# Kernel optimization log

Measured on AMD Instinct MI355X. Metric: run time of the kernel, lower is better.

The kernel has to match this reference:

```python
import jax, jax.numpy as jnp
import numpy as np

N_NODES = 100000
N_EDGES = 1600000
IN_FEATS = 256
OUT_FEATS = 128


def setup_inputs() -> dict:
    key = jax.random.key(0)
    k1, k2, k3, k4, k5 = jax.random.split(key, 5)
    feat = jax.random.normal(k1, (N_NODES, IN_FEATS), dtype=jnp.float32)
    # xavier_uniform-like init for the weight
    limit = float(np.sqrt(6.0 / (IN_FEATS + OUT_FEATS)))
    weight = jax.random.uniform(k2, (IN_FEATS, OUT_FEATS), dtype=jnp.float32,
                                minval=-limit, maxval=limit)
    edge_weight = jax.random.uniform(k3, (N_EDGES,), dtype=jnp.float32)
    src = jax.random.randint(k4, (N_EDGES,), 0, N_NODES, dtype=jnp.int64)
    dst = jax.random.randint(k5, (N_EDGES,), 0, N_NODES, dtype=jnp.int64)
    return {"feat": feat, "weight": weight, "edge_weight": edge_weight,
            "src": src, "dst": dst}


def reference(feat, weight, edge_weight, src, dst):
    N = feat.shape[0]
    ones = jnp.ones(src.shape, dtype=feat.dtype)
    # out/in degrees from edge list (clamped to >= 1), as in DGL
    out_deg = jnp.clip(jax.ops.segment_sum(ones, src, num_segments=N), 1.0)
    in_deg = jnp.clip(jax.ops.segment_sum(ones, dst, num_segments=N), 1.0)
    # norm == 'both': pre-scale sources by out_deg^-0.5
    feat_src = feat * (out_deg ** -0.5)[:, None]
    # in_feats > out_feats branch: transform (with tanh) BEFORE aggregation
    h = jnp.tanh(feat_src @ weight)                      # [N, out]
    # message = u_mul_e: h[src] * edge_weight, then sum per destination
    m = h[src] * edge_weight[:, None]                    # [E, out]
    rst = jax.ops.segment_sum(m, dst, num_segments=N)    # [N, out]
    # norm == 'both': post-scale by in_deg^-0.5
    rst = rst * (in_deg ** -0.5)[:, None]
    return rst
```

## Files before the change

kernel.cpp:

```cpp
#include <hip/hip_runtime.h>
#include <hip/hip_fp16.h>
#include <math.h>

#define N_NODES 100000
#define N_EDGES 1600000
#define IN_F 256
#define OUT_F 128
#define SCAN_TPB 256
#define SCAN_EPB 1024

#define HR 4
#define HRANGE 25000
#define HC 64
#define HCHUNK 25000
#define PWORDS (N_NODES / 2)

typedef _Float16 h8 __attribute__((ext_vector_type(8)));
typedef float f4 __attribute__((ext_vector_type(4)));

__global__ __launch_bounds__(256) void hist_kernel(
        const int* __restrict__ src, const int* __restrict__ dst,
        int* __restrict__ rank, unsigned int* __restrict__ partial_in,
        unsigned int* __restrict__ partial_out) {
    __shared__ unsigned int bins[HRANGE / 2];
    int b = blockIdx.x;
    int c = b >> 3;
    int tr = b & 7;
    int type = tr >> 2;
    int r = tr & 3;
    for (int i = threadIdx.x; i < HRANGE / 2; i += 256) bins[i] = 0;
    __syncthreads();
    const int* nodes = type ? src : dst;
    const int e0 = c * HCHUNK;
    const int lo = r * HRANGE;
    const int ngroups = HCHUNK / 4;
    for (int g = threadIdx.x; g < ngroups; g += 256) {
        int e = e0 + g * 4;
        int4 n4 = *(const int4*)(nodes + e);
        int nn[4] = {n4.x, n4.y, n4.z, n4.w};
        #pragma unroll
        for (int j = 0; j < 4; ++j) {
            unsigned loc = (unsigned)(nn[j] - lo);
            if (loc < (unsigned)HRANGE) {
                unsigned sh = (loc & 1) * 16;
                unsigned old = atomicAdd(&bins[loc >> 1], 1u << sh);
                if (type == 0) rank[e + j] = (int)((old >> sh) & 0xffffu);
            }
        }
    }
    __syncthreads();
    unsigned int* part = type ? partial_out : partial_in;
    unsigned int* dstp = part + (size_t)c * PWORDS + (lo >> 1);
    for (int i = threadIdx.x; i < HRANGE / 2; i += 256) dstp[i] = bins[i];
}

__global__ __launch_bounds__(256) void fused_reduce_kernel(
        const unsigned int* __restrict__ partial_in,
        const unsigned int* __restrict__ partial_out,
        unsigned short* __restrict__ chunk_base16,
        int* __restrict__ deg_in, float* __restrict__ rs_out,
        int* __restrict__ spart, int N) {
    __shared__ int tmp[256];
    int t = threadIdx.x;
    int n0 = blockIdx.x * SCAN_EPB + t * 4;
    int run[4] = {0, 0, 0, 0};
    int sout[4] = {0, 0, 0, 0};
    if (n0 < N) {
        const int w0 = n0 >> 1;
        #pragma unroll 4
        for (int c = 0; c < HC; ++c) {
            ushort4 cb;
            cb.x = (unsigned short)run[0]; cb.y = (unsigned short)run[1];
            cb.z = (unsigned short)run[2]; cb.w = (unsigned short)run[3];
            *(ushort4*)(chunk_base16 + (size_t)c * N_NODES + n0) = cb;
            uint2 pi = *(const uint2*)(partial_in + (size_t)c * PWORDS + w0);
            run[0] += (int)(pi.x & 0xffffu);  run[1] += (int)(pi.x >> 16);
            run[2] += (int)(pi.y & 0xffffu);  run[3] += (int)(pi.y >> 16);
            uint2 po = *(const uint2*)(partial_out + (size_t)c * PWORDS + w0);
            sout[0] += (int)(po.x & 0xffffu); sout[1] += (int)(po.x >> 16);
            sout[2] += (int)(po.y & 0xffffu); sout[3] += (int)(po.y >> 16);
        }
        *(int4*)(deg_in + n0) = make_int4(run[0], run[1], run[2], run[3]);
        float4 rs;
        rs.x = rsqrtf((float)(sout[0] < 1 ? 1 : sout[0]));
        rs.y = rsqrtf((float)(sout[1] < 1 ? 1 : sout[1]));
        rs.z = rsqrtf((float)(sout[2] < 1 ? 1 : sout[2]));
        rs.w = rsqrtf((float)(sout[3] < 1 ? 1 : sout[3]));
        *(float4*)(rs_out + n0) = rs;
    }
    tmp[t] = run[0] + run[1] + run[2] + run[3];
    __syncthreads();
    for (int off = 128; off > 0; off >>= 1) {
        if (t < off) tmp[t] += tmp[t + off];
        __syncthreads();
    }
    if (t == 0) spart[blockIdx.x] = tmp[0];
}

__global__ __launch_bounds__(128) void scan_part2(const int* __restrict__ partials,
                                                  int* __restrict__ bases, int nb) {
    __shared__ int tmp[128];
    int t = threadIdx.x;
    int v = (t < nb) ? partials[t] : 0;
    tmp[t] = v;
    __syncthreads();
    int x = v;
    for (int off = 1; off < 128; off <<= 1) {
        int y = (t >= off) ? tmp[t - off] : 0;
        __syncthreads();
        x += y;
        tmp[t] = x;
        __syncthreads();
    }
    if (t < nb) bases[t] = x - v;
}

__global__ __launch_bounds__(SCAN_TPB) void scan_part3(const int* __restrict__ deg,
                                                       const int* __restrict__ bases,
                                                       int* __restrict__ row_ptr, int N) {
    __shared__ int tmp[SCAN_TPB];
    int t = threadIdx.x;
    int i0 = blockIdx.x * SCAN_EPB + t * 4;
    int v[4];
    int s = 0;
    #pragma unroll
    for (int j = 0; j < 4; ++j) { v[j] = (i0 + j < N) ? deg[i0 + j] : 0; s += v[j]; }
    tmp[t] = s;
    __syncthreads();
    int x = s;
    for (int off = 1; off < SCAN_TPB; off <<= 1) {
        int y = (t >= off) ? tmp[t - off] : 0;
        __syncthreads();
        x += y;
        tmp[t] = x;
        __syncthreads();
    }
    int excl = bases[blockIdx.x] + x - s;
    #pragma unroll
    for (int j = 0; j < 4; ++j) {
        if (i0 + j < N) row_ptr[i0 + j] = excl;
        excl += v[j];
    }
    if (blockIdx.x == gridDim.x - 1 && t == SCAN_TPB - 1) row_ptr[N] = bases[blockIdx.x] + x;
}

__global__ __launch_bounds__(256) void fill_kernel(
        const int* __restrict__ src, const int* __restrict__ dst,
        const float* __restrict__ ew, const int* __restrict__ row_ptr,
        const unsigned short* __restrict__ chunk_base16,
        const int* __restrict__ rank, int2* __restrict__ ed, int E) {
    int e0 = (blockIdx.x * 256 + threadIdx.x) * 4;
    if (e0 >= E) return;
    int4 s4 = *(const int4*)(src + e0);
    int4 d4 = *(const int4*)(dst + e0);
    float4 w4 = *(const float4*)(ew + e0);
    int4 r4 = *(const int4*)(rank + e0);
    int c = e0 / HCHUNK;
    const unsigned short* cb = chunk_base16 + (size_t)c * N_NODES;
    int dd[4] = {d4.x, d4.y, d4.z, d4.w};
    int ss[4] = {s4.x, s4.y, s4.z, s4.w};
    int rr[4] = {r4.x, r4.y, r4.z, r4.w};
    float ww[4] = {w4.x, w4.y, w4.z, w4.w};
    #pragma unroll
    for (int j = 0; j < 4; ++j) {
        int d = dd[j];
        int p = row_ptr[d] + (int)cb[d] + rr[j];
        unsigned long long v = (unsigned long long)(unsigned int)ss[j] |
                               ((unsigned long long)(unsigned int)__float_as_int(ww[j]) << 32);
        __builtin_nontemporal_store(v, (unsigned long long*)&ed[p]);
    }
}

__global__ void wt_kernel(const float* __restrict__ W, _Float16* __restrict__ Wt) {
    int i = blockIdx.x * blockDim.x + threadIdx.x;
    if (i < IN_F * OUT_F) {
        int n = i >> 8;
        int k = i & 255;
        Wt[i] = (_Float16)W[k * OUT_F + n];
    }
}

__global__ __launch_bounds__(256) void gemm_mfma_kernel(
        const float* __restrict__ feat, const _Float16* __restrict__ Wt,
        const float* __restrict__ rs_out, __half* __restrict__ h, int N) {
    const int wave = threadIdx.x >> 6;
    const int lane = threadIdx.x & 63;
    const int m = lane & 15;
    const int quad = lane >> 4;
    const int n0 = wave * 32;

    h8 b[2][8];
    #pragma unroll
    for (int t = 0; t < 2; ++t)
        #pragma unroll
        for (int k = 0; k < 8; ++k)
            b[t][k] = *(const h8*)&Wt[(size_t)(n0 + t * 16 + m) * IN_F + k * 32 + quad * 8];

    const int rowbase = blockIdx.x * 64;

    #pragma unroll
    for (int pair = 0; pair < 2; ++pair) {
        const int r0 = rowbase + pair * 32;
        int ar0 = r0 + m;       if (ar0 >= N) ar0 = 0;
        int ar1 = r0 + 16 + m;  if (ar1 >= N) ar1 = 0;
        const float* ap0 = feat + (size_t)ar0 * IN_F + quad * 8;
        const float* ap1 = feat + (size_t)ar1 * IN_F + quad * 8;

        f4 acc00 = {0.f, 0.f, 0.f, 0.f}, acc01 = {0.f, 0.f, 0.f, 0.f};
        f4 acc10 = {0.f, 0.f, 0.f, 0.f}, acc11 = {0.f, 0.f, 0.f, 0.f};

        #pragma unroll
        for (int k = 0; k < 8; ++k) {
            float4 f00 = *(const float4*)(ap0 + k * 32);
            float4 f01 = *(const float4*)(ap0 + k * 32 + 4);
            float4 f10 = *(const float4*)(ap1 + k * 32);
            float4 f11 = *(const float4*)(ap1 + k * 32 + 4);
            h8 a0, a1;
            a0[0] = (_Float16)f00.x; a0[1] = (_Float16)f00.y;
            a0[2] = (_Float16)f00.z; a0[3] = (_Float16)f00.w;
            a0[4] = (_Float16)f01.x; a0[5] = (_Float16)f01.y;
            a0[6] = (_Float16)f01.z; a0[7] = (_Float16)f01.w;
            a1[0] = (_Float16)f10.x; a1[1] = (_Float16)f10.y;
            a1[2] = (_Float16)f10.z; a1[3] = (_Float16)f10.w;
            a1[4] = (_Float16)f11.x; a1[5] = (_Float16)f11.y;
            a1[6] = (_Float16)f11.z; a1[7] = (_Float16)f11.w;
            acc00 = __builtin_amdgcn_mfma_f32_16x16x32_f16(a0, b[0][k], acc00, 0, 0, 0);
            acc01 = __builtin_amdgcn_mfma_f32_16x16x32_f16(a0, b[1][k], acc01, 0, 0, 0);
            acc10 = __builtin_amdgcn_mfma_f32_16x16x32_f16(a1, b[0][k], acc10, 0, 0, 0);
            acc11 = __builtin_amdgcn_mfma_f32_16x16x32_f16(a1, b[1][k], acc11, 0, 0, 0);
        }

        #pragma unroll
        for (int tile = 0; tile < 2; ++tile) {
            const f4 aL = tile ? acc10 : acc00;
            const f4 aR = tile ? acc11 : acc01;
            const int crow = r0 + tile * 16 + quad * 4;
            #pragma unroll
            for (int r = 0; r < 4; ++r) {
                const int rr = crow + r;
                if (rr < N) {
                    const float rs = rs_out[rr];
                    h[(size_t)rr * OUT_F + n0 + m]      = __float2half(tanhf(aL[r] * rs));
                    h[(size_t)rr * OUT_F + n0 + 16 + m] = __float2half(tanhf(aR[r] * rs));
                }
            }
        }
    }
}

__global__ __launch_bounds__(256) void gather_kernel(
        const __half* __restrict__ h, const int2* __restrict__ ed,
        const int* __restrict__ row_ptr, float* __restrict__ out, int N) {
    int wave = threadIdx.x >> 6;
    int lane = threadIdx.x & 63;
    int node = blockIdx.x * 4 + wave;
    if (node >= N) return;
    int lo = row_ptr[node];
    int hi = row_ptr[node + 1];
    int p = lane >> 4;
    int c = lane & 15;
    float acc[4][8];
    #pragma unroll
    for (int g = 0; g < 4; ++g)
        #pragma unroll
        for (int i = 0; i < 8; ++i) acc[g][i] = 0.f;

    for (int j = lo; j < hi; j += 16) {
        #pragma unroll
        for (int g = 0; g < 4; ++g) {
            int jj = j + g * 4 + p;
            int2 e = (jj < hi) ? ed[jj] : make_int2(0, 0);
            float w = __int_as_float(e.y);
            int4 rrow = *(const int4*)(h + (size_t)e.x * OUT_F + c * 8);
            float2 t;
            t = __half22float2(*(__half2*)&rrow.x); acc[g][0] += w * t.x; acc[g][1] += w * t.y;
            t = __half22float2(*(__half2*)&rrow.y); acc[g][2] += w * t.x; acc[g][3] += w * t.y;
            t = __half22float2(*(__half2*)&rrow.z); acc[g][4] += w * t.x; acc[g][5] += w * t.y;
            t = __half22float2(*(__half2*)&rrow.w); acc[g][6] += w * t.x; acc[g][7] += w * t.y;
        }
    }
    float v[8];
    #pragma unroll
    for (int i = 0; i < 8; ++i) {
        v[i] = (acc[0][i] + acc[1][i]) + (acc[2][i] + acc[3][i]);
        v[i] += __shfl_xor(v[i], 16);
        v[i] += __shfl_xor(v[i], 32);
    }
    if (p == 0) {
        int deg = hi - lo; if (deg < 1) deg = 1;
        float rs = rsqrtf((float)deg);
        float* op = out + (size_t)node * OUT_F + c * 8;
        *(float4*)op       = make_float4(v[0] * rs, v[1] * rs, v[2] * rs, v[3] * rs);
        *(float4*)(op + 4) = make_float4(v[4] * rs, v[5] * rs, v[6] * rs, v[7] * rs);
    }
}

extern "C" void kernel_launch(void* const* d_in, const int* in_sizes, int n_in,
                              void* d_out, int out_size, void* d_ws, size_t ws_size,
                              hipStream_t stream) {
    const float* feat   = (const float*)d_in[0];
    const float* weight = (const float*)d_in[1];
    const float* ew     = (const float*)d_in[2];
    const int*   src    = (const int*)d_in[3];
    const int*   dst    = (const int*)d_in[4];
    float* out = (float*)d_out;

    char* ws = (char*)d_ws;
    float* rs_out      = (float*)(ws);
    int*   deg_in      = (int*)(ws + 400000);
    int*   row_ptr     = (int*)(ws + 800000);
    int*   spart       = (int*)(ws + 1200016);
    int*   sbases      = (int*)(ws + 1200528);
    int*   rank        = (int*)(ws + 1201056);
    unsigned int* partial_in  = (unsigned int*)(ws + 7601056);
    int2*  ed          = (int2*)(ws + 7601056);
    unsigned short* chunk_base16 = (unsigned short*)(ws + 20401056);
    unsigned int* partial_out = (unsigned int*)(ws + 33201056);
    __half* h          = (__half*)(ws + 20401056);
    _Float16* Wt       = (_Float16*)(ws + 46001056);

    const int nb = (N_NODES + SCAN_EPB - 1) / SCAN_EPB;

    hist_kernel<<<2 * HR * HC, 256, 0, stream>>>(src, dst, rank, partial_in, partial_out);
    fused_reduce_kernel<<<nb, 256, 0, stream>>>(partial_in, partial_out, chunk_base16,
                                                deg_in, rs_out, spart, N_NODES);
    scan_part2<<<1, 128, 0, stream>>>(spart, sbases, nb);
    scan_part3<<<nb, SCAN_TPB, 0, stream>>>(deg_in, sbases, row_ptr, N_NODES);
    fill_kernel<<<(N_EDGES / 4 + 255) / 256, 256, 0, stream>>>(src, dst, ew, row_ptr,
                                                               chunk_base16, rank, ed, N_EDGES);
    wt_kernel<<<(IN_F * OUT_F + 255) / 256, 256, 0, stream>>>(weight, Wt);
    gemm_mfma_kernel<<<(N_NODES + 63) / 64, 256, 0, stream>>>(feat, Wt, rs_out, h, N_NODES);
    gather_kernel<<<(N_NODES + 3) / 4, 256, 0, stream>>>(h, ed, row_ptr, out, N_NODES);
}
```

Baseline: 403.0 us.

## Stage GEMM weights in swizzled LDS and process 128 rows per block

The fp16 transposed weight matrix (64 KB) is now copied into LDS with an XOR swizzle, instead of each wave holding 16 h8 B fragments in registers. Each block now handles 128 rows, as two halves of 64 rows with four A tiles per wave, which halves the number of blocks and spreads the weight load over more rows. B fragments are read from LDS on every k step. The goal is lower register pressure (launch bounds 256,2) and more rows in flight per wave to hide feat loads, at the cost of a 64 KB LDS footprint that limits occupancy and a per-block weight staging prologue.

```diff
diff --git a/kernel.cpp b/kernel.cpp
--- a/kernel.cpp
+++ b/kernel.cpp
@@ -14,6 +14,8 @@
 #define HC 64
 #define HCHUNK 25000
 #define PWORDS (N_NODES / 2)
+
+#define GM_ROWS 128
 
 typedef _Float16 h8 __attribute__((ext_vector_type(8)));
 typedef float f4 __attribute__((ext_vector_type(4)));
@@ -180,42 +182,72 @@
     }
 }
 
-__global__ __launch_bounds__(256) void gemm_mfma_kernel(
+__global__ __launch_bounds__(256, 2) void gemm_mfma_kernel(
         const float* __restrict__ feat, const _Float16* __restrict__ Wt,
         const float* __restrict__ rs_out, __half* __restrict__ h, int N) {
-    const int wave = threadIdx.x >> 6;
-    const int lane = threadIdx.x & 63;
+    __shared__ _Float16 wlds[OUT_F * IN_F];
+    const int tid = threadIdx.x;
+
+    for (int gi = tid; gi < OUT_F * IN_F / 8; gi += 256) {
+        int row = gi >> 5;
+        int gc  = gi & 31;
+        int gs  = gc ^ (row & 7);
+        *(int4*)&wlds[(size_t)(row * 32 + gs) * 8] = *(const int4*)&Wt[(size_t)gi * 8];
+    }
+    __syncthreads();
+
+    const int wave = tid >> 6;
+    const int lane = tid & 63;
     const int m = lane & 15;
     const int quad = lane >> 4;
     const int n0 = wave * 32;
 
-    h8 b[2][8];
-    #pragma unroll
-    for (int t = 0; t < 2; ++t)
-        #pragma unroll
-        for (int k = 0; k < 8; ++k)
-            b[t][k] = *(const h8*)&Wt[(size_t)(n0 + t * 16 + m) * IN_F + k * 32 + quad * 8];
-
-    const int rowbase = blockIdx.x * 64;
-
-    #pragma unroll
-    for (int pair = 0; pair < 2; ++pair) {
-        const int r0 = rowbase + pair * 32;
-        int ar0 = r0 + m;       if (ar0 >= N) ar0 = 0;
-        int ar1 = r0 + 16 + m;  if (ar1 >= N) ar1 = 0;
-        const float* ap0 = feat + (size_t)ar0 * IN_F + quad * 8;
-        const float* ap1 = feat + (size_t)ar1 * IN_F + quad * 8;
-
-        f4 acc00 = {0.f, 0.f, 0.f, 0.f}, acc01 = {0.f, 0.f, 0.f, 0.f};
-        f4 acc10 = {0.f, 0.f, 0.f, 0.f}, acc11 = {0.f, 0.f, 0.f, 0.f};
+    const int rowbase = blockIdx.x * GM_ROWS;
+    const int brow0 = n0 + m;
+    const int brow1 = n0 + 16 + m;
+
+    #pragma unroll
+    for (int half = 0; half < 2; ++half) {
+        const int r0 = rowbase + half * 64;
+        const float* ap0;
+        const float* ap1;
+        const float* ap2;
+        const float* ap3;
+        {
+            int a0 = r0 + m;       if (a0 >= N) a0 = 0;
+            int a1 = r0 + 16 + m;  if (a1 >= N) a1 = 0;
+            int a2 = r0 + 32 + m;  if (a2 >= N) a2 = 0;
+            int a3 = r0 + 48 + m;  if (a3 >= N) a3 = 0;
+            ap0 = feat + (size_t)a0 * IN_F + quad * 8;
+            ap1 = feat + (size_t)a1 * IN_F + quad * 8;
+            ap2 = feat + (size_t)a2 * IN_F + quad * 8;
+            ap3 = feat + (size_t)a3 * IN_F + quad * 8;
+        }
+
+        f4 acc[4][2];
+        #pragma unroll
+        for (int t = 0; t < 4; ++t) {
+            acc[t][0] = (f4){0.f, 0.f, 0.f, 0.f};
+            acc[t][1] = (f4){0.f, 0.f, 0.f, 0.f};
+        }
 
         #pragma unroll
         for (int k = 0; k < 8; ++k) {
+            const int gc0 = (k * 4 + quad) ^ (brow0 & 7);
+            const int gc1 = (k * 4 + quad) ^ (brow1 & 7);
+            h8 b0 = *(const h8*)&wlds[(size_t)(brow0 * 32 + gc0) * 8];
+            h8 b1 = *(const h8*)&wlds[(size_t)(brow1 * 32 + gc1) * 8];
+
             float4 f00 = *(const float4*)(ap0 + k * 32);
             float4 f01 = *(const float4*)(ap0 + k * 32 + 4);
             float4 f10 = *(const float4*)(ap1 + k * 32);
             float4 f11 = *(const float4*)(ap1 + k * 32 + 4);
-            h8 a0, a1;
+            float4 f20 = *(const float4*)(ap2 + k * 32);
+            float4 f21 = *(const float4*)(ap2 + k * 32 + 4);
+            float4 f30 = *(const float4*)(ap3 + k * 32);
+            float4 f31 = *(const float4*)(ap3 + k * 32 + 4);
+
+            h8 a0, a1, a2, a3;
             a0[0] = (_Float16)f00.x; a0[1] = (_Float16)f00.y;
             a0[2] = (_Float16)f00.z; a0[3] = (_Float16)f00.w;
             a0[4] = (_Float16)f01.x; a0[5] = (_Float16)f01.y;
@@ -224,24 +256,35 @@
             a1[2] = (_Float16)f10.z; a1[3] = (_Float16)f10.w;
             a1[4] = (_Float16)f11.x; a1[5] = (_Float16)f11.y;
             a1[6] = (_Float16)f11.z; a1[7] = (_Float16)f11.w;
-            acc00 = __builtin_amdgcn_mfma_f32_16x16x32_f16(a0, b[0][k], acc00, 0, 0, 0);
-            acc01 = __builtin_amdgcn_mfma_f32_16x16x32_f16(a0, b[1][k], acc01, 0, 0, 0);
-            acc10 = __builtin_amdgcn_mfma_f32_16x16x32_f16(a1, b[0][k], acc10, 0, 0, 0);
-            acc11 = __builtin_amdgcn_mfma_f32_16x16x32_f16(a1, b[1][k], acc11, 0, 0, 0);
-        }
-
-        #pragma unroll
-        for (int tile = 0; tile < 2; ++tile) {
-            const f4 aL = tile ? acc10 : acc00;
-            const f4 aR = tile ? acc11 : acc01;
-            const int crow = r0 + tile * 16 + quad * 4;
+            a2[0] = (_Float16)f20.x; a2[1] = (_Float16)f20.y;
+            a2[2] = (_Float16)f20.z; a2[3] = (_Float16)f20.w;
+            a2[4] = (_Float16)f21.x; a2[5] = (_Float16)f21.y;
+            a2[6] = (_Float16)f21.z; a2[7] = (_Float16)f21.w;
+            a3[0] = (_Float16)f30.x; a3[1] = (_Float16)f30.y;
+            a3[2] = (_Float16)f30.z; a3[3] = (_Float16)f30.w;
+            a3[4] = (_Float16)f31.x; a3[5] = (_Float16)f31.y;
+            a3[6] = (_Float16)f31.z; a3[7] = (_Float16)f31.w;
+
+            acc[0][0] = __builtin_amdgcn_mfma_f32_16x16x32_f16(a0, b0, acc[0][0], 0, 0, 0);
+            acc[0][1] = __builtin_amdgcn_mfma_f32_16x16x32_f16(a0, b1, acc[0][1], 0, 0, 0);
+            acc[1][0] = __builtin_amdgcn_mfma_f32_16x16x32_f16(a1, b0, acc[1][0], 0, 0, 0);
+            acc[1][1] = __builtin_amdgcn_mfma_f32_16x16x32_f16(a1, b1, acc[1][1], 0, 0, 0);
+            acc[2][0] = __builtin_amdgcn_mfma_f32_16x16x32_f16(a2, b0, acc[2][0], 0, 0, 0);
+            acc[2][1] = __builtin_amdgcn_mfma_f32_16x16x32_f16(a2, b1, acc[2][1], 0, 0, 0);
+            acc[3][0] = __builtin_amdgcn_mfma_f32_16x16x32_f16(a3, b0, acc[3][0], 0, 0, 0);
+            acc[3][1] = __builtin_amdgcn_mfma_f32_16x16x32_f16(a3, b1, acc[3][1], 0, 0, 0);
+        }
+
+        #pragma unroll
+        for (int t = 0; t < 4; ++t) {
+            const int crow = r0 + t * 16 + quad * 4;
             #pragma unroll
             for (int r = 0; r < 4; ++r) {
                 const int rr = crow + r;
                 if (rr < N) {
                     const float rs = rs_out[rr];
-                    h[(size_t)rr * OUT_F + n0 + m]      = __float2half(tanhf(aL[r] * rs));
-                    h[(size_t)rr * OUT_F + n0 + 16 + m] = __float2half(tanhf(aR[r] * rs));
+                    h[(size_t)rr * OUT_F + n0 + m]      = __float2half(tanhf(acc[t][0][r] * rs));
+                    h[(size_t)rr * OUT_F + n0 + 16 + m] = __float2half(tanhf(acc[t][1][r] * rs));
                 }
             }
         }
@@ -329,6 +372,6 @@
     fill_kernel<<<(N_EDGES / 4 + 255) / 256, 256, 0, stream>>>(src, dst, ew, row_ptr,
                                                                chunk_base16, rank, ed, N_EDGES);
     wt_kernel<<<(IN_F * OUT_F + 255) / 256, 256, 0, stream>>>(weight, Wt);
-    gemm_mfma_kernel<<<(N_NODES + 63) / 64, 256, 0, stream>>>(feat, Wt, rs_out, h, N_NODES);
+    gemm_mfma_kernel<<<(N_NODES + GM_ROWS - 1) / GM_ROWS, 256, 0, stream>>>(feat, Wt, rs_out, h, N_NODES);
     gather_kernel<<<(N_NODES + 3) / 4, 256, 0, stream>>>(h, ed, row_ptr, out, N_NODES);
 }
```

Measured after the change: 412.9 us. 1.02x slower.
